# Performance work log

Measured on AMD Instinct MI355X. Metric: run time of the kernel, lower is better.

The kernel has to match this reference:

```python
import jax, jax.numpy as jnp
import numpy as np

MAX_LEN = 4096
D_MODEL = 768
POS_EMBED_DIM = 65
MLP_WIDTH = 64
NUM_LAYERS = 2
ORDER = 2
BATCH = 4
FAST_DECAY_PCT = 0.3
SLOW_DECAY_PCT = 1.5
TARGET = 0.01
SHIFT = 0.0


def make_z(l):
    # PosEmbeddings.z_init: (l, 1 + 2*bands)
    bands = (POS_EMBED_DIM - 1) // 2
    t = jnp.linspace(0.0, 1.0, MAX_LEN)[:l, None]
    t_rescaled = jnp.linspace(0.0, MAX_LEN - 1, MAX_LEN)[:l, None]
    w = 2 * jnp.pi * t_rescaled / l
    f = jnp.linspace(1e-4, bands - 1, bands)[None]
    zc = jnp.exp(-1j * f * w)
    return jnp.concatenate([t, zc.real, zc.imag], axis=-1).astype(jnp.float32)


def fftconv(seq, filt, bias):
    # seq: (b, l, d); filt: (l, d); bias: (d,)
    seq_len = seq.shape[-2]
    fft_size = 2 * seq_len
    filter_f = jnp.fft.rfft(filt, n=fft_size, axis=-2) / fft_size
    seq_f = jnp.fft.rfft(seq, n=fft_size, axis=-2)
    y = jnp.fft.irfft(seq_f * filter_f, n=fft_size, norm='forward', axis=-2)[..., :seq_len, :]
    return y + seq * bias


def setup_inputs() -> dict:
    key = jax.random.key(0)
    ks = jax.random.split(key, 8)
    s_mlp = 1.0 / np.sqrt(MLP_WIDTH)
    s_in = 1.0 / np.sqrt(POS_EMBED_DIM)
    s_d = 1.0 / np.sqrt(D_MODEL)
    s_p = 1.0 / np.sqrt((ORDER + 1) * D_MODEL)
    return {
        'u': jax.random.normal(ks[0], (BATCH, MAX_LEN, D_MODEL), jnp.float32),
        'z': make_z(MAX_LEN),
        'fin_W': jax.random.normal(ks[1], (POS_EMBED_DIM, MLP_WIDTH), jnp.float32) * s_in,
        'fin_b': jnp.zeros((MLP_WIDTH,), jnp.float32),
        'freq': jnp.full((MLP_WIDTH,), 1.0, jnp.float32),
        'mid_W': jax.random.normal(ks[2], (NUM_LAYERS, MLP_WIDTH, MLP_WIDTH), jnp.float32) * s_mlp,
        'mid_b': jnp.zeros((NUM_LAYERS, MLP_WIDTH), jnp.float32),
        'fout_W': jax.random.normal(ks[3], (MLP_WIDTH, (ORDER - 1) * D_MODEL), jnp.float32) * s_mlp,
        'proj_W': jax.random.normal(ks[4], (D_MODEL, (ORDER + 1) * D_MODEL), jnp.float32) * s_d,
        'proj_b': jnp.zeros(((ORDER + 1) * D_MODEL,), jnp.float32),
        'conv_W': jax.random.normal(ks[5], (3, (ORDER + 1) * D_MODEL), jnp.float32) * 0.3,
        'conv_b': jnp.zeros(((ORDER + 1) * D_MODEL,), jnp.float32),
        'filt_bias': jax.random.normal(ks[6], (ORDER - 1, D_MODEL), jnp.float32),
        'out_W': jax.random.normal(ks[7], ((ORDER + 1) * D_MODEL // (ORDER + 1) * (ORDER + 1), D_MODEL), jnp.float32)[: (ORDER + 1) * D_MODEL // (ORDER + 1) * 0 + (ORDER + 1) * D_MODEL // (ORDER + 1), :] * 0 + jax.random.normal(ks[7], (D_MODEL, D_MODEL), jnp.float32) * s_d,
        'out_b': jnp.zeros((D_MODEL,), jnp.float32),
    }


def reference(u, z, fin_W, fin_b, freq, mid_W, mid_b, fout_W, proj_W, proj_b, conv_W, conv_b, filt_bias, out_W, out_b):
    l = min(u.shape[-2], MAX_LEN)
    t = jnp.linspace(0.0, 1.0, MAX_LEN)[:l, None]  # (l, 1)

    # HyenaFilter: implicit filter MLP with sine activations
    k = jnp.sin(freq * (z @ fin_W + fin_b))
    for i in range(NUM_LAYERS):
        k = jnp.sin(freq * (k @ mid_W[i] + mid_b[i]))
    k = k @ fout_W  # (l, (order-1)*d)
    filters = k.reshape(l, ORDER - 1, D_MODEL).transpose(1, 0, 2)  # (o, l, d)

    # ExponentialModulation
    max_decay = jnp.log(TARGET) / FAST_DECAY_PCT
    min_decay = jnp.log(TARGET) / SLOW_DECAY_PCT
    deltas = jnp.linspace(min_decay, max_decay, D_MODEL)
    decay = jnp.exp(-t * jnp.abs(deltas))  # (l, d)
    filters = filters * (decay + SHIFT)

    # input projection + depthwise causal conv (kernel 3)
    up = u @ proj_W + proj_b  # (b, l, 3d)
    pad = jnp.pad(up, ((0, 0), (2, 0), (0, 0)))
    uc = conv_W[0] * pad[:, :l] + conv_W[1] * pad[:, 1:l + 1] + conv_W[2] * pad[:, 2:l + 2] + conv_b

    parts = jnp.split(uc, ORDER + 1, axis=-1)
    x, v = parts[:-1], parts[-1]
    for o in range(ORDER - 1):
        v = fftconv(v * x[o], filters[o], filt_bias[o])
    y = (v * x[-1]) @ out_W + out_b
    return y
```

## Files before the change

### kernel.cpp

```cpp
#include <hip/hip_runtime.h>
#include <math.h>

#define MAX_LEN 4096
#define D_MODEL 768
#define PE_DIM 65
#define MLP_W 64
#define NBATCH 4
#define D3 2304
#define ROWS (NBATCH*MAX_LEN)

typedef unsigned short u16;
typedef unsigned int u32;
typedef float f4 __attribute__((ext_vector_type(4)));
typedef __bf16 bf16x8 __attribute__((ext_vector_type(8)));
typedef float f32x4 __attribute__((ext_vector_type(4)));

__device__ inline u16 f2bf(float x) {
    u32 u = __float_as_uint(x);
    u += 0x7fffu + ((u >> 16) & 1u);
    return (u16)(u >> 16);
}
__device__ inline float bf2f(u16 v) { return __uint_as_float((u32)v << 16); }
__device__ inline u32 pk2(float a, float b) {
    return (u32)f2bf(a) | ((u32)f2bf(b) << 16);
}

#define GLDS16(gp, lp) __builtin_amdgcn_global_load_lds( \
    (const __attribute__((address_space(1))) u32*)(gp), \
    (__attribute__((address_space(3))) u32*)(lp), 16, 0, 0)

__launch_bounds__(256)
__global__ void filter_mlp_kernel(const float* __restrict__ z,
                                  const float* __restrict__ fin_W,
                                  const float* __restrict__ fin_b,
                                  const float* __restrict__ freq,
                                  const float* __restrict__ mid_W,
                                  const float* __restrict__ mid_b,
                                  float* __restrict__ k3out)
{
    __shared__ __align__(16) float W1[PE_DIM*MLP_W];
    __shared__ __align__(16) float Wm[2*MLP_W*MLP_W];
    __shared__ __align__(16) float zs[16*PE_DIM];
    __shared__ __align__(16) float kb[2][16*MLP_W];
    int tid = threadIdx.x;
    int t0 = blockIdx.x * 16;
    for (int i = tid; i < PE_DIM*MLP_W; i += 256) W1[i] = fin_W[i];
    for (int i = tid; i < 2*MLP_W*MLP_W; i += 256) Wm[i] = mid_W[i];
    for (int i = tid; i < 16*PE_DIM; i += 256) zs[i] = z[(size_t)t0*PE_DIM + i];
    __syncthreads();

    int j = tid & 63, tl = tid >> 6;
    float fj = freq[j];
    float a[4];

    {
        float fb = fin_b[j];
        #pragma unroll
        for (int tt = 0; tt < 4; ++tt) a[tt] = fb;
        for (int i = 0; i < PE_DIM; ++i) {
            float w = W1[i*MLP_W + j];
            #pragma unroll
            for (int tt = 0; tt < 4; ++tt)
                a[tt] += zs[(tl + 4*tt)*PE_DIM + i] * w;
        }
        #pragma unroll
        for (int tt = 0; tt < 4; ++tt)
            kb[0][(tl + 4*tt)*MLP_W + j] = sinf(fj*a[tt]);
    }
    __syncthreads();
    {
        float mb = mid_b[j];
        #pragma unroll
        for (int tt = 0; tt < 4; ++tt) a[tt] = mb;
        for (int i = 0; i < MLP_W; ++i) {
            float w = Wm[i*MLP_W + j];
            #pragma unroll
            for (int tt = 0; tt < 4; ++tt)
                a[tt] += kb[0][(tl + 4*tt)*MLP_W + i] * w;
        }
        #pragma unroll
        for (int tt = 0; tt < 4; ++tt)
            kb[1][(tl + 4*tt)*MLP_W + j] = sinf(fj*a[tt]);
    }
    __syncthreads();
    {
        float mb = mid_b[MLP_W + j];
        #pragma unroll
        for (int tt = 0; tt < 4; ++tt) a[tt] = mb;
        for (int i = 0; i < MLP_W; ++i) {
            float w = Wm[MLP_W*MLP_W + i*MLP_W + j];
            #pragma unroll
            for (int tt = 0; tt < 4; ++tt)
                a[tt] += kb[1][(tl + 4*tt)*MLP_W + i] * w;
        }
        #pragma unroll
        for (int tt = 0; tt < 4; ++tt)
            k3out[(size_t)(t0 + tl + 4*tt)*MLP_W + j] = sinf(fj*a[tt]);
    }
}

__launch_bounds__(256)
__global__ void filter_out_kernel(const float* __restrict__ k3,
                                  const float* __restrict__ fout_W,
                                  float* __restrict__ hTt)
{
    __shared__ __align__(16) float ks[64*64];
    __shared__ __align__(16) float fs[64*132];
    int tid = threadIdx.x;
    int d0 = blockIdx.x * 128;
    int t0 = blockIdx.y * 64;

    for (int q = tid; q < 1024; q += 256)
        *(f4*)&ks[q*4] = *(const f4*)&k3[(size_t)t0*MLP_W + q*4];
    for (int q = tid; q < 2048; q += 256) {
        int i = q >> 5, c = q & 31;
        *(f4*)&fs[i*132 + c*4] = *(const f4*)&fout_W[(size_t)i*D_MODEL + d0 + c*4];
    }
    __syncthreads();

    int c = tid & 31;
    int t_base = (tid >> 5)*8;
    f4 acc[8];
    #pragma unroll
    for (int tt = 0; tt < 8; ++tt) acc[tt] = (f4){0.f,0.f,0.f,0.f};

    for (int i = 0; i < MLP_W; ++i) {
        f4 fv = *(const f4*)&fs[i*132 + c*4];
        #pragma unroll
        for (int tt = 0; tt < 8; ++tt) {
            float kv = ks[(t_base + tt)*MLP_W + i];
            acc[tt][0] += kv * fv[0];
            acc[tt][1] += kv * fv[1];
            acc[tt][2] += kv * fv[2];
            acc[tt][3] += kv * fv[3];
        }
    }

    const float MIND = -3.0701134573253944f;
    const float MAXD = -15.350567286626972f;
    #pragma unroll
    for (int tt = 0; tt < 8; ++tt) {
        int t = t0 + t_base + tt;
        float ttf = (float)t * (1.0f/(float)(MAX_LEN-1));
        f4 o;
        #pragma unroll
        for (int dd = 0; dd < 4; ++dd) {
            int d = d0 + 4*c + dd;
            float delta = MIND + (MAXD-MIND)*((float)d*(1.0f/(float)(D_MODEL-1)));
            o[dd] = acc[tt][dd] * expf(-ttf*fabsf(delta));
        }
        *(f4*)&hTt[(size_t)t*D_MODEL + d0 + 4*c] = o;
    }
}

__global__ void cast_bf16_kernel(const float* __restrict__ src,
                                 u16* __restrict__ dst, int n)
{
    int i = (blockIdx.x*256 + threadIdx.x)*8;
    if (i + 7 >= n) {
        for (int j = i; j < n; ++j) dst[j] = f2bf(src[j]);
        return;
    }
    float4 a = *(const float4*)(src + i);
    float4 b = *(const float4*)(src + i + 4);
    uint4 o;
    o.x = pk2(a.x, a.y);
    o.y = pk2(a.z, a.w);
    o.z = pk2(b.x, b.y);
    o.w = pk2(b.z, b.w);
    *(uint4*)(dst + i) = o;
}

__global__ void transpose_cast_kernel(const float* __restrict__ src,
                                      u16* __restrict__ dst, int R, int C)
{
    __shared__ u16 tile[64][65];
    int c0 = blockIdx.x*64, r0 = blockIdx.y*64;
    int tid = threadIdx.x;
    #pragma unroll
    for (int p = 0; p < 16; ++p) {
        int idx = tid + 256*p;
        int rr = idx >> 6, cc = idx & 63;
        tile[rr][cc] = f2bf(src[(size_t)(r0+rr)*C + c0 + cc]);
    }
    __syncthreads();
    #pragma unroll
    for (int p = 0; p < 16; ++p) {
        int idx = tid + 256*p;
        int cr = idx >> 6, rc = idx & 63;
        dst[(size_t)(c0+cr)*R + r0 + rc] = tile[rc][cr];
    }
}

__launch_bounds__(512, 2)
__global__ void gemm_mfma256_kernel(const u16* __restrict__ A,
                                    const u16* __restrict__ Bt,
                                    const float* __restrict__ bias,
                                    float* __restrict__ C,
                                    int M, int N, int K)
{
    __shared__ __align__(16) u16 lds[65536];

    int nwg = gridDim.x * gridDim.y;
    int bid = blockIdx.y * gridDim.x + blockIdx.x;
    int cpx = nwg >> 3;
    int swz = (bid & 7) * cpx + (bid >> 3);
    int bx = swz % gridDim.x, by = swz / gridDim.x;
    int m0 = by * 256, n0 = bx * 256;

    int tid = threadIdx.x;
    int lane = tid & 63, w = tid >> 6;
    int lrow = lane & 15, lch = lane >> 4;
    int wm = (w >> 2) * 128;
    int wn = (w & 3) * 64;

    int srow = 32*w + (lane >> 2);
    int scol = (lane & 3)*8;
    const u16* baseA = A  + (size_t)(m0 + srow)*K + scol;
    const u16* baseB = Bt + (size_t)(n0 + srow)*K + scol;

    auto stageA = [&](int kt_, int kk_) {
        u16* dst = lds + (size_t)(((kt_ & 1) << 15) + (kk_ << 13) + (w << 10));
        const u16* src = baseA + (size_t)kt_*64 + (size_t)kk_*32;
        GLDS16(src, dst);
        GLDS16(src + 16*(size_t)K, dst + 512);
    };
    auto stageB = [&](int kt_, int kk_) {
        u16* dst = lds + (size_t)(16384 + ((kt_ & 1) << 15) + (kk_ << 13) + (w << 10));
        const u16* src = baseB + (size_t)kt_*64 + (size_t)kk_*32;
        GLDS16(src, dst);
        GLDS16(src + 16*(size_t)K, dst + 512);
    };

    f32x4 acc[8][4];
    #pragma unroll
    for (int i = 0; i < 8; ++i)
        #pragma unroll
        for (int j = 0; j < 4; ++j)
            acc[i][j] = (f32x4){0.f,0.f,0.f,0.f};

    int NT = K >> 6;

    stageA(0, 0); stageB(0, 0);
    stageA(0, 1); stageB(0, 1);
    stageA(1, 0); stageB(1, 0);

    bf16x8 bfr[4];

#define PHASE(mh, kk, STAGE_STMT, LOADB)                                        \
    {                                                                           \
        __builtin_amdgcn_s_barrier();                                           \
        asm volatile("" ::: "memory");                                          \
        STAGE_STMT;                                                             \
        bf16x8 af[4];                                                           \
        _Pragma("unroll")                                                       \
        for (int i = 0; i < 4; ++i)                                             \
            af[i] = *(const bf16x8*)&lds[bsel + ((kk) << 13)                    \
                     + (wm + (mh)*64 + i*16 + lrow)*32 + lch*8];                \
        if (LOADB) {                                                            \
            _Pragma("unroll")                                                   \
            for (int j = 0; j < 4; ++j)                                         \
                bfr[j] = *(const bf16x8*)&lds[bsel + 16384 + ((kk) << 13)       \
                          + (wn + j*16 + lrow)*32 + lch*8];                     \
        }                                                                       \
        __builtin_amdgcn_s_setprio(1);                                          \
        _Pragma("unroll")                                                       \
        for (int i = 0; i < 4; ++i)                                             \
            _Pragma("unroll")                                                   \
            for (int j = 0; j < 4; ++j)                                         \
                acc[(mh)*4 + i][j] = __builtin_amdgcn_mfma_f32_16x16x32_bf16(   \
                    af[i], bfr[j], acc[(mh)*4 + i][j], 0, 0, 0);                \
        __builtin_amdgcn_s_setprio(0);                                          \
    }

    #pragma unroll 1
    for (int kt = 0; kt < NT; ++kt) {
        const int bsel = (kt & 1) << 15;
        if (kt < NT - 1) asm volatile("s_waitcnt vmcnt(4)" ::: "memory");
        else             asm volatile("s_waitcnt vmcnt(0)" ::: "memory");
        PHASE(0, 0, if (kt + 1 < NT) stageA(kt + 1, 1), 1)
        PHASE(1, 0, if (kt + 1 < NT) stageB(kt + 1, 1), 0)
        PHASE(0, 1, if (kt + 2 < NT) stageA(kt + 2, 0), 1)
        PHASE(1, 1, if (kt + 2 < NT) stageB(kt + 2, 0), 0)
    }
#undef PHASE

    #pragma unroll
    for (int nt = 0; nt < 4; ++nt) {
        int n = n0 + wn + nt*16 + lrow;
        float bv = bias[n];
        #pragma unroll
        for (int mt = 0; mt < 8; ++mt) {
            int m = m0 + wm + mt*16 + lch*4;
            #pragma unroll
            for (int r = 0; r < 4; ++r)
                C[(size_t)(m + r)*N + n] = acc[mt][nt][r] + bv;
        }
    }
}

__global__ void convprep_kernel(const float* __restrict__ up,
                                const float* __restrict__ conv_W,
                                const float* __restrict__ conv_b,
                                u16* __restrict__ seqbf,
                                float* __restrict__ gate)
{
    __shared__ float sb[64][65];
    int d0 = blockIdx.x * 64;
    int t0 = blockIdx.y * 64;
    int b  = blockIdx.z;
    int tid = threadIdx.x;
    #pragma unroll
    for (int i = 0; i < 16; ++i) {
        int idx = tid + 256*i;
        int trow = idx >> 6, dcol = idx & 63;
        int t = t0 + trow;
        int d = d0 + dcol;
        size_t r = ((size_t)b*MAX_LEN + t)*D3;
        float uc[3];
        #pragma unroll
        for (int g = 0; g < 3; ++g) {
            int c = d + g*D_MODEL;
            float u0 = up[r + c];
            float u1 = (t >= 1) ? up[r - D3 + c]   : 0.f;
            float u2 = (t >= 2) ? up[r - 2*D3 + c] : 0.f;
            uc[g] = conv_W[c]*u2 + conv_W[D3 + c]*u1 + conv_W[2*D3 + c]*u0 + conv_b[c];
        }
        sb[trow][dcol] = uc[0]*uc[2];
        gate[((size_t)b*MAX_LEN + t)*D_MODEL + d] = uc[1];
    }
    __syncthreads();
    #pragma unroll
    for (int i = 0; i < 16; ++i) {
        int idx = tid + 256*i;
        int drow = idx >> 6, tcol = idx & 63;
        seqbf[((size_t)b*D_MODEL + d0 + drow)*MAX_LEN + t0 + tcol] = f2bf(sb[tcol][drow]);
    }
}

__launch_bounds__(256)
__global__ void longconv_mfma_kernel(const u16* __restrict__ seqbf,
                                     const u16* __restrict__ hbf,
                                     const float* __restrict__ filt_bias,
                                     float* __restrict__ yT)
{
    __shared__ __align__(16) u16 sq[4*4896];
    __shared__ __align__(16) u16 hp[4112];
    __shared__ __align__(16) u16 A_s[16*648];

    int d   = blockIdx.x;
    int tid = threadIdx.x;
    int lane = tid & 63, w = tid >> 6;
    int lrow = lane & 15, lch = lane >> 4;

    for (int q = tid; q < 4*544; q += 256) {
        int b = q / 544, qq = q - b*544;
        int p = b*4896 + ((qq + (qq >> 3)) << 3);
        uint4 o = make_uint4(0u,0u,0u,0u);
        if (qq >= 32) o = *(const uint4*)&seqbf[((size_t)b*D_MODEL + d)*MAX_LEN + (size_t)(qq-32)*8];
        *(uint4*)&sq[p] = o;
    }
    for (int q = tid; q < 514; q += 256) {
        uint4 o = make_uint4(0u,0u,0u,0u);
        if (q >= 2) o = *(const uint4*)&hbf[(size_t)d*MAX_LEN + (size_t)(q-2)*8];
        *(uint4*)&hp[q*8] = o;
    }

    f32x4 acc[16];
    #pragma unroll
    for (int g = 0; g < 16; ++g) acc[g] = (f32x4){0.f,0.f,0.f,0.f};

    int slab_b = tid >> 4;
    int i_b    = tid & 15;
    int rot    = (slab_b & 3)*4;
    u32* bld = (u32*)&A_s[slab_b*648 + i_b*40];

    const char* sqb = (const char*)(sq + w*4896);
    int Q0 = 30 + 2*lrow + lch;

#define MM(af_, bf_, gi) acc[gi] = __builtin_amdgcn_mfma_f32_16x16x32_bf16(af_, bf_, acc[gi], 0, 0, 0)

    #pragma unroll 1
    for (int s = 0; s < 8; ++s) {
        __syncthreads();
        {
            int hbase = 32 + 256*slab_b + 32*s + i_b;
            #pragma unroll
            for (int j = 0; j < 16; ++j) {
                int kk = (j + rot) & 15;
                u16 v0 = hp[hbase - 2*kk];
                u16 v1 = hp[hbase - 2*kk - 1];
                bld[kk] = (u32)v0 | ((u32)v1 << 16);
            }
        }
        __syncthreads();
        bf16x8 aR[16];
        #pragma unroll
        for (int r = 0; r < 16; ++r)
            aR[r] = *(const bf16x8*)&A_s[r*648 + lrow*40 + lch*8];
        int Qs = Q0 - 4*s;
        const char* bp = sqb + (Qs*16 + (Qs >> 3)*16);
        #pragma unroll
        for (int dlt = 0; dlt < 16; ++dlt) {
            bf16x8 F = *(const bf16x8*)(bp + 576*dlt);
            #pragma unroll
            for (int r = 0; r < 16 - dlt; ++r)
                MM(aR[r], F, r + dlt);
        }
    }
#undef MM

    float fb = filt_bias[d];
    const u16* sqbu = sq + w*4896;
    float* dsty = yT + ((size_t)w*D_MODEL + d)*MAX_LEN;
    #pragma unroll
    for (int g = 0; g < 16; ++g) {
        int t0 = 256*g + 16*lrow + 4*lch;
        int elem = 256 + t0;
        int Q = elem >> 3;
        const u16* pv = &sqbu[(((Q + (Q >> 3)) << 3)) | (elem & 7)];
        ushort4 sv = *(const ushort4*)pv;
        f4 o;
        o[0] = acc[g][0] + fb*bf2f(sv.x);
        o[1] = acc[g][1] + fb*bf2f(sv.y);
        o[2] = acc[g][2] + fb*bf2f(sv.z);
        o[3] = acc[g][3] + fb*bf2f(sv.w);
        *(f4*)&dsty[t0] = o;
    }
}

__global__ void gatemul_kernel(const float* __restrict__ yT,
                               const float* __restrict__ gate,
                               u16* __restrict__ Afin)
{
    __shared__ float tb[64][65];
    int d0 = blockIdx.x * 64;
    int t0 = blockIdx.y * 64;
    int b  = blockIdx.z;
    int tid = threadIdx.x;
    #pragma unroll
    for (int i = 0; i < 16; ++i) {
        int idx = tid + 256*i;
        int drow = idx >> 6, tcol = idx & 63;
        tb[drow][tcol] = yT[((size_t)b*D_MODEL + d0 + drow)*MAX_LEN + t0 + tcol];
    }
    __syncthreads();
    #pragma unroll
    for (int i = 0; i < 16; ++i) {
        int idx = tid + 256*i;
        int trow = idx >> 6, dcol = idx & 63;
        size_t r = ((size_t)b*MAX_LEN + t0 + trow)*D_MODEL + d0 + dcol;
        Afin[r] = f2bf(tb[dcol][trow] * gate[r]);
    }
}

extern "C" void kernel_launch(void* const* d_in, const int* in_sizes, int n_in,
                              void* d_out, int out_size, void* d_ws, size_t ws_size,
                              hipStream_t stream)
{
    (void)in_sizes; (void)n_in; (void)out_size; (void)ws_size;
    const float* u      = (const float*)d_in[0];
    const float* z      = (const float*)d_in[1];
    const float* fin_W  = (const float*)d_in[2];
    const float* fin_b  = (const float*)d_in[3];
    const float* freq   = (const float*)d_in[4];
    const float* mid_W  = (const float*)d_in[5];
    const float* mid_b  = (const float*)d_in[6];
    const float* fout_W = (const float*)d_in[7];
    const float* proj_W = (const float*)d_in[8];
    const float* proj_b = (const float*)d_in[9];
    const float* conv_W = (const float*)d_in[10];
    const float* conv_b = (const float*)d_in[11];
    const float* fbias  = (const float*)d_in[12];
    const float* out_W  = (const float*)d_in[13];
    const float* out_b  = (const float*)d_in[14];
    float* out = (float*)d_out;

    float* ws    = (float*)d_ws;
    u16*   hbf   = (u16*)ws;
    float* up    = ws + 1572864;
    float* gate  = up + 37748736;
    u16*   seqbf = (u16*)(gate + 12582912);
    u16*   Abf   = (u16*)(gate + 12582912 + 6291456);
    u16*   BpT1  = (u16*)(gate + 12582912 + 2*6291456);
    u16*   BpT2  = (u16*)(gate + 12582912 + 2*6291456 + 884736);
    float* hTt   = up;
    float* yT    = up;
    u16*   Afinbf= (u16*)(up + 16777216);
    float* k3buf = gate;

    filter_mlp_kernel<<<MAX_LEN/16, 256, 0, stream>>>(z, fin_W, fin_b, freq,
                                                      mid_W, mid_b, k3buf);
    filter_out_kernel<<<dim3(D_MODEL/128, MAX_LEN/64), 256, 0, stream>>>(
        k3buf, fout_W, hTt);
    transpose_cast_kernel<<<dim3(D_MODEL/64, MAX_LEN/64), 256, 0, stream>>>(
        hTt, hbf, MAX_LEN, D_MODEL);
    cast_bf16_kernel<<<(ROWS*D_MODEL)/(256*8), 256, 0, stream>>>(u, Abf, ROWS*D_MODEL);
    transpose_cast_kernel<<<dim3(D3/64, D_MODEL/64), 256, 0, stream>>>(
        proj_W, BpT1, D_MODEL, D3);
    gemm_mfma256_kernel<<<dim3(D3/256, ROWS/256), 512, 0, stream>>>(
        Abf, BpT1, proj_b, up, ROWS, D3, D_MODEL);
    convprep_kernel<<<dim3(D_MODEL/64, MAX_LEN/64, NBATCH), 256, 0, stream>>>(
        up, conv_W, conv_b, seqbf, gate);
    transpose_cast_kernel<<<dim3(D_MODEL/64, D_MODEL/64), 256, 0, stream>>>(
        out_W, BpT2, D_MODEL, D_MODEL);
    longconv_mfma_kernel<<<D_MODEL, 256, 0, stream>>>(seqbf, hbf, fbias, yT);
    gatemul_kernel<<<dim3(D_MODEL/64, MAX_LEN/64, NBATCH), 256, 0, stream>>>(
        yT, gate, Afinbf);
    gemm_mfma256_kernel<<<dim3(D_MODEL/256, ROWS/256), 512, 0, stream>>>(
        Afinbf, BpT2, out_b, out, ROWS, D_MODEL, D_MODEL);
}
```

Measured before the change: 403.2 us.

## Swizzle LDS tile layout and reorder GEMM barriers/staging per phase

Applies an XOR swizzle to the 16-byte chunk index when staging A/B tiles into LDS and when reading fragments, to reduce LDS bank conflicts on the ds_read path. It also restructures each phase so fragment reads come first, then the next global-to-LDS stage is issued, the vmcnt wait moves to the end of the last phase, and barriers are placed around the MFMA block. This changes the synchronisation schedule and adds extra barriers per phase, which could cost some latency, in exchange for overlapping loads with compute.

Measured after the change: 396.0 us. Within noise of the previous version (-1.8%).

```diff
diff --git a/kernel.cpp b/kernel.cpp
--- a/kernel.cpp
+++ b/kernel.cpp
@@ -213,9 +213,10 @@
     int lrow = lane & 15, lch = lane >> 4;
     int wm = (w >> 2) * 128;
     int wn = (w & 3) * 64;
+    int lchx8 = (lch ^ ((lrow >> 1) & 3)) * 8;
 
     int srow = 32*w + (lane >> 2);
-    int scol = (lane & 3)*8;
+    int scol = ((lane & 3) ^ ((lane >> 3) & 3))*8;
     const u16* baseA = A  + (size_t)(m0 + srow)*K + scol;
     const u16* baseB = Bt + (size_t)(n0 + srow)*K + scol;
 
@@ -244,25 +245,29 @@
     stageA(0, 0); stageB(0, 0);
     stageA(0, 1); stageB(0, 1);
     stageA(1, 0); stageB(1, 0);
+    asm volatile("s_waitcnt vmcnt(4)" ::: "memory");
+    __builtin_amdgcn_s_barrier();
+    asm volatile("" ::: "memory");
 
     bf16x8 bfr[4];
 
-#define PHASE(mh, kk, STAGE_STMT, LOADB)                                        \
+#define PHASE(mh, kk, STAGE_STMT, LOADB, WAIT_STMT)                             \
     {                                                                           \
-        __builtin_amdgcn_s_barrier();                                           \
-        asm volatile("" ::: "memory");                                          \
-        STAGE_STMT;                                                             \
         bf16x8 af[4];                                                           \
         _Pragma("unroll")                                                       \
         for (int i = 0; i < 4; ++i)                                             \
             af[i] = *(const bf16x8*)&lds[bsel + ((kk) << 13)                    \
-                     + (wm + (mh)*64 + i*16 + lrow)*32 + lch*8];                \
+                     + (wm + (mh)*64 + i*16 + lrow)*32 + lchx8];                \
         if (LOADB) {                                                            \
             _Pragma("unroll")                                                   \
             for (int j = 0; j < 4; ++j)                                         \
                 bfr[j] = *(const bf16x8*)&lds[bsel + 16384 + ((kk) << 13)       \
-                          + (wn + j*16 + lrow)*32 + lch*8];                     \
+                          + (wn + j*16 + lrow)*32 + lchx8];                     \
         }                                                                       \
+        STAGE_STMT;                                                             \
+        WAIT_STMT;                                                              \
+        asm volatile("" ::: "memory");                                          \
+        __builtin_amdgcn_s_barrier();                                           \
         __builtin_amdgcn_s_setprio(1);                                          \
         _Pragma("unroll")                                                       \
         for (int i = 0; i < 4; ++i)                                             \
@@ -271,17 +276,23 @@
                 acc[(mh)*4 + i][j] = __builtin_amdgcn_mfma_f32_16x16x32_bf16(   \
                     af[i], bfr[j], acc[(mh)*4 + i][j], 0, 0, 0);                \
         __builtin_amdgcn_s_setprio(0);                                          \
+        __builtin_amdgcn_s_barrier();                                           \
+        asm volatile("" ::: "memory");                                          \
     }
 
     #pragma unroll 1
     for (int kt = 0; kt < NT; ++kt) {
         const int bsel = (kt & 1) << 15;
-        if (kt < NT - 1) asm volatile("s_waitcnt vmcnt(4)" ::: "memory");
-        else             asm volatile("s_waitcnt vmcnt(0)" ::: "memory");
-        PHASE(0, 0, if (kt + 1 < NT) stageA(kt + 1, 1), 1)
-        PHASE(1, 0, if (kt + 1 < NT) stageB(kt + 1, 1), 0)
-        PHASE(0, 1, if (kt + 2 < NT) stageA(kt + 2, 0), 1)
-        PHASE(1, 1, if (kt + 2 < NT) stageB(kt + 2, 0), 0)
+        PHASE(0, 0, if (kt + 1 < NT) stageA(kt + 1, 1), 1, )
+        PHASE(1, 0, if (kt + 1 < NT) stageB(kt + 1, 1), 0, )
+        PHASE(0, 1, if (kt + 2 < NT) stageA(kt + 2, 0), 1, )
+        if (kt < NT - 2) {
+            PHASE(1, 1, stageB(kt + 2, 0), 0,
+                  asm volatile("s_waitcnt vmcnt(4)" ::: "memory"))
+        } else {
+            PHASE(1, 1, , 0,
+                  asm volatile("s_waitcnt vmcnt(0)" ::: "memory"))
+        }
     }
 #undef PHASE
 
```
